# Kernel optimization log

Measured on AMD Instinct MI355X. Metric: run time of the kernel, lower is better.

## Reference

```python
import jax, jax.numpy as jnp
import numpy as np

N = 1_000_000   # samples
D_IN = 100      # covariate dim (cfg_density[0][0])
H = 64          # hidden dim
NUM_HEADS = 5   # t-bins [0,.2,.4,.6,.8,1.0]


def setup_inputs() -> dict:
    key = jax.random.key(0)
    ks = jax.random.split(key, 17)
    s = 0.05  # param scale for numerical stability (torch init is data-independent anyway)
    return {
        "t": jax.random.uniform(ks[0], (N,), dtype=jnp.float32),
        "x": jax.random.normal(ks[1], (N, D_IN), dtype=jnp.float32),
        # density feature MLP (two Linear+ReLU layers)
        "dW1": jax.random.normal(ks[2], (D_IN, H), dtype=jnp.float32) * s,
        "db1": jax.random.normal(ks[3], (H,), dtype=jnp.float32) * s,
        "dW2": jax.random.normal(ks[4], (H, H), dtype=jnp.float32) * s,
        "db2": jax.random.normal(ks[5], (H,), dtype=jnp.float32) * s,
        # 5 multi-head branches, each 3 Treat_Linear layers (istreat=1 since isenhance=1)
        "hw1": jax.random.normal(ks[6], (NUM_HEADS, H, H), dtype=jnp.float32) * s,
        "htw1": jax.random.normal(ks[7], (NUM_HEADS, H), dtype=jnp.float32) * s,
        "hb1": jax.random.normal(ks[8], (NUM_HEADS, H), dtype=jnp.float32) * s,
        "hw2": jax.random.normal(ks[9], (NUM_HEADS, H, H), dtype=jnp.float32) * s,
        "htw2": jax.random.normal(ks[10], (NUM_HEADS, H), dtype=jnp.float32) * s,
        "hb2": jax.random.normal(ks[11], (NUM_HEADS, H), dtype=jnp.float32) * s,
        "hw3": jax.random.normal(ks[12], (NUM_HEADS, H, 1), dtype=jnp.float32) * s,
        "htw3": jax.random.normal(ks[13], (NUM_HEADS, 1), dtype=jnp.float32) * s,
        "hb3": jax.random.normal(ks[14], (NUM_HEADS, 1), dtype=jnp.float32) * s,
    }


def reference(t, x, dW1, db1, dW2, db2,
              hw1, htw1, hb1, hw2, htw2, hb2, hw3, htw3, hb3):
    # hidden_features: Linear+ReLU, Linear+ReLU
    h = jax.nn.relu(x @ dW1 + db1)        # [N, H]
    h = jax.nn.relu(h @ dW2 + db2)        # [N, H]

    tt = t[:, None]                        # treatment column [N, 1]
    # bin index per row: t in [0.2*q, 0.2*(q+1)); last bin closed at 1.0
    bins = jnp.clip(jnp.floor(t * NUM_HEADS).astype(jnp.int32), 0, NUM_HEADS - 1)

    out = jnp.zeros((x.shape[0], 1), dtype=h.dtype)
    for q in range(NUM_HEADS):  # fixed small set of structurally-distinct heads
        # Treat_Linear layer 1: feat@W + t*tw + b, relu
        a = jax.nn.relu(h @ hw1[q] + tt * htw1[q] + hb1[q])
        # Treat_Linear layer 2
        a = jax.nn.relu(a @ hw2[q] + tt * htw2[q] + hb2[q])
        # last layer: no activation, islastlayer=1
        a = a @ hw3[q] + tt * htw3[q] + hb3[q]   # [N, 1]
        out = out + jnp.where((bins == q)[:, None], a, 0.0)
    return out  # Drnet returns (None, Q); g is None so we return Q
```

## Files before the change

### kernel.cpp

```cpp
#include <hip/hip_runtime.h>

typedef _Float16 f16;
typedef _Float16 f16x8 __attribute__((ext_vector_type(8)));
typedef float f32x4 __attribute__((ext_vector_type(4)));

#define NB 5
#define H 64
#define DIN 100
#define NT 256
#define MAIN_BLOCKS 512

#define FR_W1   0
#define FR_W2   1024
#define FR_HD   1536
#define FR_TOT  6656

__global__ __launch_bounds__(256)
void prepack_kernel(const float* __restrict__ dW1, const float* __restrict__ dW2,
                    const float* __restrict__ hw1, const float* __restrict__ hw2,
                    f16x8* __restrict__ pw)
{
    int F = blockIdx.x * 256 + threadIdx.x;
    if (F >= FR_TOT) return;
    int lane = F & 63, g = lane >> 4, c = lane & 15;
    const float* src;
    int s, mt, kmax;
    if (F < FR_W2) {
        int r = F; s = r >> 8; mt = (r >> 6) & 3; src = dW1; kmax = 100;
    } else if (F < FR_HD) {
        int r = F - FR_W2; s = r >> 8; mt = (r >> 6) & 3; src = dW2; kmax = 64;
    } else {
        int r = F - FR_HD; int ql = r >> 9; int q = ql >> 1; int l = ql & 1;
        int r2 = r & 511; s = r2 >> 8; mt = (r2 >> 6) & 3;
        src = (l ? hw2 : hw1) + q * 64 * 64; kmax = 64;
    }
    f16x8 v;
    #pragma unroll
    for (int e = 0; e < 8; ++e) {
        int k = 32 * s + 8 * g + e;
        int m = 16 * mt + c;
        float val = (k < kmax) ? src[k * 64 + m] : 0.0f;
        v[e] = (f16)val;
    }
    pw[F] = v;
}

__device__ __forceinline__ f32x4 mfma16(f16x8 a, f16x8 b, f32x4 c) {
    return __builtin_amdgcn_mfma_f32_16x16x32_f16(a, b, c, 0, 0, 0);
}

__device__ __forceinline__ void epi_plain(unsigned char* buf, int row, int g,
                                          const f32x4* acc, const float* bias) {
    #pragma unroll
    for (int mt = 0; mt < 4; ++mt) {
        const float* bb = &bias[16 * mt + 4 * g];
        union { f16 h[4]; unsigned long long u; } pk;
        #pragma unroll
        for (int r2 = 0; r2 < 4; ++r2) pk.h[r2] = (f16)fmaxf(acc[mt][r2] + bb[r2], 0.f);
        *(unsigned long long*)(buf + ((row * 128 + 32 * mt + 8 * g) ^ ((row & 7) << 4))) = pk.u;
    }
}

__device__ __forceinline__ void epi_t(unsigned char* buf, int row, int g, float rt,
                                      const f32x4* acc, const float* bias, const float* tw) {
    #pragma unroll
    for (int mt = 0; mt < 4; ++mt) {
        const float* bb = &bias[16 * mt + 4 * g];
        const float* tt = &tw[16 * mt + 4 * g];
        union { f16 h[4]; unsigned long long u; } pk;
        #pragma unroll
        for (int r2 = 0; r2 < 4; ++r2)
            pk.h[r2] = (f16)fmaxf(acc[mt][r2] + bb[r2] + rt * tt[r2], 0.f);
        *(unsigned long long*)(buf + ((row * 128 + 32 * mt + 8 * g) ^ ((row & 7) << 4))) = pk.u;
    }
}

__device__ __forceinline__ f16x8 lds_read_h(const unsigned char* buf, int row, int g, int s) {
    return *(const f16x8*)(buf + ((row * 128 + 64 * s + 16 * g) ^ ((row & 7) << 4)));
}

__global__ __launch_bounds__(NT, 2)
void drnet_main(const float* __restrict__ t, const float* __restrict__ x,
                const float* __restrict__ db1, const float* __restrict__ db2,
                const float* __restrict__ hb1, const float* __restrict__ htw1,
                const float* __restrict__ hb2, const float* __restrict__ htw2,
                const float* __restrict__ hw3, const float* __restrict__ htw3,
                const float* __restrict__ hb3,
                const f16x8* __restrict__ pw,
                float* __restrict__ out, int N, int nch)
{
    __shared__ float sb1f[H], sb2f[H];
    __shared__ float shb1[NB * H], shw1t[NB * H], shb2[NB * H], shw2t[NB * H], sw3f[NB * H];
    __shared__ float shtw3[NB], shb3[NB];
    __shared__ unsigned char sli[NT], sqv[NT];
    __shared__ float stv[NT];
    __shared__ float sout[NT];
    __shared__ int scnt[NB + 1], sbase[NB + 1];
    __shared__ __align__(16) unsigned char hbuf[4][2][2][2048];

    const int tid = threadIdx.x;
    const int lane = tid & 63;
    const int wv = tid >> 6;
    const int g = lane >> 4;
    const int row = lane & 15;

    for (int p = tid; p < H; p += NT) { sb1f[p] = db1[p]; sb2f[p] = db2[p]; }
    for (int p = tid; p < NB * H; p += NT) {
        shb1[p] = hb1[p];  shw1t[p] = htw1[p];
        shb2[p] = hb2[p];  shw2t[p] = htw2[p];
        sw3f[p] = hw3[p];
    }
    if (tid < NB) { shtw3[tid] = htw3[tid]; shb3[tid] = hb3[tid]; }

    f16x8 w1f[16], w2f[8];
    #pragma unroll
    for (int u = 0; u < 16; ++u) w1f[u] = pw[FR_W1 + u * 64 + lane];
    #pragma unroll
    for (int u = 0; u < 8; ++u)  w2f[u] = pw[FR_W2 + u * 64 + lane];

    float tpre = 0.f;
    {
        int i0 = blockIdx.x * NT + tid;
        if (blockIdx.x < nch && i0 < N) tpre = t[i0];
    }

    for (int ch = blockIdx.x; ch < nch; ch += MAIN_BLOCKS) {
        if (tid <= NB) scnt[tid] = 0;
        __syncthreads();
        const int i0 = ch * NT + tid;
        const float tv0 = tpre;
        int q0 = NB;
        if (i0 < N) q0 = min((int)(tv0 * 5.0f), NB - 1);
        int pos = atomicAdd(&scnt[q0], 1);
        __syncthreads();
        if (tid == 0) {
            int r = 0;
            #pragma unroll
            for (int b = 0; b <= NB; ++b) { sbase[b] = r; r += scnt[b]; }
        }
        __syncthreads();
        int sp = sbase[q0] + pos;
        sli[sp] = (unsigned char)tid; sqv[sp] = (unsigned char)q0; stv[sp] = tv0;
        __syncthreads();

        {
            int inx = (ch + MAIN_BLOCKS) * NT + tid;
            tpre = (ch + MAIN_BLOCKS < nch && inx < N) ? t[inx] : 0.f;
        }

        for (int j = 0; j < 2; ++j) {
            const int pA = (wv * 4 + 2 * j) * 16;
            const int pB = pA + 16;
            const int qloA = sqv[pA];
            const int qloB = sqv[pB];
            const int liA = sli[pA + row], liB = sli[pB + row];
            const int rqA = sqv[pA + row], rqB = sqv[pB + row];
            const float rtA = stv[pA + row], rtB = stv[pB + row];
            const int ivA = (rqA < NB) ? (ch * NT + liA) : (ch * NT);
            const int ivB = (rqB < NB) ? (ch * NT + liB) : (ch * NT);

            float4 xrA[7], xrB[7];
            {
                const float4* x4 = (const float4*)(x + (size_t)ivA * DIN);
                #pragma unroll
                for (int s = 0; s < 3; ++s) { xrA[2*s] = x4[8*s + 2*g]; xrA[2*s+1] = x4[8*s + 2*g + 1]; }
                xrA[6] = x4[24];
            }
            {
                const float4* x4 = (const float4*)(x + (size_t)ivB * DIN);
                #pragma unroll
                for (int s = 0; s < 3; ++s) { xrB[2*s] = x4[8*s + 2*g]; xrB[2*s+1] = x4[8*s + 2*g + 1]; }
                xrB[6] = x4[24];
            }

            if (qloA >= NB) continue;

            f16x8 xfA[4], xfB[4];
            #pragma unroll
            for (int s = 0; s < 3; ++s) {
                float4 a = xrA[2*s], b = xrA[2*s+1];
                xfA[s][0]=(f16)a.x; xfA[s][1]=(f16)a.y; xfA[s][2]=(f16)a.z; xfA[s][3]=(f16)a.w;
                xfA[s][4]=(f16)b.x; xfA[s][5]=(f16)b.y; xfA[s][6]=(f16)b.z; xfA[s][7]=(f16)b.w;
                float4 c = xrB[2*s], d = xrB[2*s+1];
                xfB[s][0]=(f16)c.x; xfB[s][1]=(f16)c.y; xfB[s][2]=(f16)c.z; xfB[s][3]=(f16)c.w;
                xfB[s][4]=(f16)d.x; xfB[s][5]=(f16)d.y; xfB[s][6]=(f16)d.z; xfB[s][7]=(f16)d.w;
            }
            {
                const bool lo = (g == 0);
                float4 a = xrA[6], b = xrB[6];
                xfA[3][0]=lo?(f16)a.x:(f16)0.f; xfA[3][1]=lo?(f16)a.y:(f16)0.f;
                xfA[3][2]=lo?(f16)a.z:(f16)0.f; xfA[3][3]=lo?(f16)a.w:(f16)0.f;
                xfA[3][4]=(f16)0.f; xfA[3][5]=(f16)0.f; xfA[3][6]=(f16)0.f; xfA[3][7]=(f16)0.f;
                xfB[3][0]=lo?(f16)b.x:(f16)0.f; xfB[3][1]=lo?(f16)b.y:(f16)0.f;
                xfB[3][2]=lo?(f16)b.z:(f16)0.f; xfB[3][3]=lo?(f16)b.w:(f16)0.f;
                xfB[3][4]=(f16)0.f; xfB[3][5]=(f16)0.f; xfB[3][6]=(f16)0.f; xfB[3][7]=(f16)0.f;
            }

            const f32x4 zero = {0.f, 0.f, 0.f, 0.f};
            unsigned char* hA_A = hbuf[wv][0][0];
            unsigned char* hB_A = hbuf[wv][0][1];
            unsigned char* hA_B = hbuf[wv][1][0];
            unsigned char* hB_B = hbuf[wv][1][1];

            f32x4 accA[4] = {zero, zero, zero, zero};
            f32x4 accB[4] = {zero, zero, zero, zero};
            #pragma unroll
            for (int s = 0; s < 4; ++s)
                #pragma unroll
                for (int mt = 0; mt < 4; ++mt) {
                    accA[mt] = mfma16(w1f[s * 4 + mt], xfA[s], accA[mt]);
                    accB[mt] = mfma16(w1f[s * 4 + mt], xfB[s], accB[mt]);
                }
            epi_plain(hA_A, row, g, accA, sb1f);
            epi_plain(hA_B, row, g, accB, sb1f);

            f32x4 acc2A[4] = {zero, zero, zero, zero};
            f32x4 acc2B[4] = {zero, zero, zero, zero};
            #pragma unroll
            for (int s = 0; s < 2; ++s) {
                f16x8 hfA = lds_read_h(hA_A, row, g, s);
                f16x8 hfB = lds_read_h(hA_B, row, g, s);
                #pragma unroll
                for (int mt = 0; mt < 4; ++mt) {
                    acc2A[mt] = mfma16(w2f[s * 4 + mt], hfA, acc2A[mt]);
                    acc2B[mt] = mfma16(w2f[s * 4 + mt], hfB, acc2B[mt]);
                }
            }
            epi_plain(hB_A, row, g, acc2A, sb2f);
            epi_plain(hB_B, row, g, acc2B, sb2f);

            const int qhiA = min((int)sqv[pA + 15], NB - 1);
            int qhi = qhiA;
            if (qloB < NB) qhi = max(qhi, min((int)sqv[pB + 15], NB - 1));

            #pragma unroll 1
            for (int q = qloA; q <= qhi; ++q) {
                const f16x8* ph1 = pw + FR_HD + (q * 2 + 0) * 512;
                const f16x8* ph2 = pw + FR_HD + (q * 2 + 1) * 512;

                f32x4 a1A[4] = {zero, zero, zero, zero};
                f32x4 a1B[4] = {zero, zero, zero, zero};
                #pragma unroll
                for (int s = 0; s < 2; ++s) {
                    f16x8 hfA = lds_read_h(hB_A, row, g, s);
                    f16x8 hfB = lds_read_h(hB_B, row, g, s);
                    #pragma unroll
                    for (int mt = 0; mt < 4; ++mt) {
                        f16x8 wf = ph1[(s * 4 + mt) * 64 + lane];
                        a1A[mt] = mfma16(wf, hfA, a1A[mt]);
                        a1B[mt] = mfma16(wf, hfB, a1B[mt]);
                    }
                }
                epi_t(hA_A, row, g, rtA, a1A, &shb1[q * 64], &shw1t[q * 64]);
                epi_t(hA_B, row, g, rtB, a1B, &shb1[q * 64], &shw1t[q * 64]);

                f32x4 a2A[4] = {zero, zero, zero, zero};
                f32x4 a2B[4] = {zero, zero, zero, zero};
                #pragma unroll
                for (int s = 0; s < 2; ++s) {
                    f16x8 hfA = lds_read_h(hA_A, row, g, s);
                    f16x8 hfB = lds_read_h(hA_B, row, g, s);
                    #pragma unroll
                    for (int mt = 0; mt < 4; ++mt) {
                        f16x8 wf = ph2[(s * 4 + mt) * 64 + lane];
                        a2A[mt] = mfma16(wf, hfA, a2A[mt]);
                        a2B[mt] = mfma16(wf, hfB, a2B[mt]);
                    }
                }

                float pa = 0.f, pb = 0.f;
                #pragma unroll
                for (int mt = 0; mt < 4; ++mt) {
                    const float* bb = &shb2[q * 64 + 16 * mt + 4 * g];
                    const float* tw = &shw2t[q * 64 + 16 * mt + 4 * g];
                    const float* w3 = &sw3f[q * 64 + 16 * mt + 4 * g];
                    #pragma unroll
                    for (int r2 = 0; r2 < 4; ++r2) {
                        float vA = fmaxf(a2A[mt][r2] + bb[r2] + rtA * tw[r2], 0.f);
                        float vB = fmaxf(a2B[mt][r2] + bb[r2] + rtB * tw[r2], 0.f);
                        pa += vA * w3[r2];
                        pb += vB * w3[r2];
                    }
                }
                pa += __shfl_xor(pa, 16, 64);
                pa += __shfl_xor(pa, 32, 64);
                pb += __shfl_xor(pb, 16, 64);
                pb += __shfl_xor(pb, 32, 64);
                if (lane < 16) {
                    if (rqA == q) sout[liA] = pa + rtA * shtw3[q] + shb3[q];
                    if (rqB == q) sout[liB] = pb + rtB * shtw3[q] + shb3[q];
                }
            }
        }

        __syncthreads();
        {
            const int iw = ch * NT + tid;
            if (iw < N) out[iw] = sout[tid];
        }
    }
}

extern "C" void kernel_launch(void* const* d_in, const int* in_sizes, int n_in,
                              void* d_out, int out_size, void* d_ws, size_t ws_size,
                              hipStream_t stream) {
    const float* t    = (const float*)d_in[0];
    const float* x    = (const float*)d_in[1];
    const float* dW1  = (const float*)d_in[2];
    const float* db1  = (const float*)d_in[3];
    const float* dW2  = (const float*)d_in[4];
    const float* db2  = (const float*)d_in[5];
    const float* hw1  = (const float*)d_in[6];
    const float* htw1 = (const float*)d_in[7];
    const float* hb1  = (const float*)d_in[8];
    const float* hw2  = (const float*)d_in[9];
    const float* htw2 = (const float*)d_in[10];
    const float* hb2  = (const float*)d_in[11];
    const float* hw3  = (const float*)d_in[12];
    const float* htw3 = (const float*)d_in[13];
    const float* hb3  = (const float*)d_in[14];
    float* out = (float*)d_out;

    const int N = in_sizes[0];
    const int nch = (N + NT - 1) / NT;
    f16x8* pw = (f16x8*)d_ws;

    prepack_kernel<<<(FR_TOT + 255) / 256, 256, 0, stream>>>(dW1, dW2, hw1, hw2, pw);
    drnet_main<<<MAIN_BLOCKS, NT, 0, stream>>>(t, x, db1, db2, hb1, htw1, hb2, htw2,
                                               hw3, htw3, hb3, pw, out, N, nch);
}
```

Before: 160.6 us.

## Stage trunk weights in LDS and issue all four x tile loads up front

Trunk weight fragments (W1, W2) are now copied once per block into shared memory and read from LDS, instead of living in 24 f16x8 registers per lane. This frees registers so the kernel can prefetch all four 16-row x tiles per wave before any compute, giving more memory-level parallelism. The cost is 24 KB of extra LDS, which may limit occupancy, plus LDS read traffic inside the MFMA loops. Rows are loaded even for wavefronts whose tiles are empty.

```diff
diff --git a/kernel.cpp b/kernel.cpp
--- a/kernel.cpp
+++ b/kernel.cpp
@@ -14,6 +14,7 @@
 #define FR_W2   1024
 #define FR_HD   1536
 #define FR_TOT  6656
+#define FR_TRUNK 1536
 
 __global__ __launch_bounds__(256)
 void prepack_kernel(const float* __restrict__ dW1, const float* __restrict__ dW2,
@@ -45,8 +46,37 @@
     pw[F] = v;
 }
 
+struct XF { f16x8 v[4]; };
+
 __device__ __forceinline__ f32x4 mfma16(f16x8 a, f16x8 b, f32x4 c) {
     return __builtin_amdgcn_mfma_f32_16x16x32_f16(a, b, c, 0, 0, 0);
+}
+
+__device__ __forceinline__ f16x8 ldw(const unsigned char* swf, int idx) {
+    return *(const f16x8*)(swf + (idx << 4));
+}
+
+__device__ __forceinline__ void load_tile(float4* xr, const float* x, int iv, int g) {
+    const float4* x4 = (const float4*)(x + (size_t)iv * DIN);
+    #pragma unroll
+    for (int s = 0; s < 3; ++s) { xr[2*s] = x4[8*s + 2*g]; xr[2*s+1] = x4[8*s + 2*g + 1]; }
+    xr[6] = x4[24];
+}
+
+__device__ __forceinline__ void conv_tile(XF& xf, const float4* xr, int g) {
+    #pragma unroll
+    for (int s = 0; s < 3; ++s) {
+        float4 a = xr[2*s], b = xr[2*s+1];
+        xf.v[s][0]=(f16)a.x; xf.v[s][1]=(f16)a.y; xf.v[s][2]=(f16)a.z; xf.v[s][3]=(f16)a.w;
+        xf.v[s][4]=(f16)b.x; xf.v[s][5]=(f16)b.y; xf.v[s][6]=(f16)b.z; xf.v[s][7]=(f16)b.w;
+    }
+    {
+        const bool lo = (g == 0);
+        float4 a = xr[6];
+        xf.v[3][0]=lo?(f16)a.x:(f16)0.f; xf.v[3][1]=lo?(f16)a.y:(f16)0.f;
+        xf.v[3][2]=lo?(f16)a.z:(f16)0.f; xf.v[3][3]=lo?(f16)a.w:(f16)0.f;
+        xf.v[3][4]=(f16)0.f; xf.v[3][5]=(f16)0.f; xf.v[3][6]=(f16)0.f; xf.v[3][7]=(f16)0.f;
+    }
 }
 
 __device__ __forceinline__ void epi_plain(unsigned char* buf, int row, int g,
@@ -96,6 +126,7 @@
     __shared__ float stv[NT];
     __shared__ float sout[NT];
     __shared__ int scnt[NB + 1], sbase[NB + 1];
+    __shared__ __align__(16) unsigned char swf[FR_TRUNK * 16];
     __shared__ __align__(16) unsigned char hbuf[4][2][2][2048];
 
     const int tid = threadIdx.x;
@@ -111,18 +142,122 @@
         sw3f[p] = hw3[p];
     }
     if (tid < NB) { shtw3[tid] = htw3[tid]; shb3[tid] = hb3[tid]; }
-
-    f16x8 w1f[16], w2f[8];
-    #pragma unroll
-    for (int u = 0; u < 16; ++u) w1f[u] = pw[FR_W1 + u * 64 + lane];
-    #pragma unroll
-    for (int u = 0; u < 8; ++u)  w2f[u] = pw[FR_W2 + u * 64 + lane];
+    for (int p = tid; p < FR_TRUNK; p += NT)
+        ((float4*)swf)[p] = ((const float4*)pw)[p];
 
     float tpre = 0.f;
     {
         int i0 = blockIdx.x * NT + tid;
         if (blockIdx.x < nch && i0 < N) tpre = t[i0];
     }
+
+    auto compute_pair = [&](const XF& xfA, const XF& xfB, int pA) {
+        const int qloA = sqv[pA];
+        if (qloA >= NB) return;
+        const int pB = pA + 16;
+        const int qloB = sqv[pB];
+        const int liA = sli[pA + row], liB = sli[pB + row];
+        const int rqA = sqv[pA + row], rqB = sqv[pB + row];
+        const float rtA = stv[pA + row], rtB = stv[pB + row];
+
+        const f32x4 zero = {0.f, 0.f, 0.f, 0.f};
+        unsigned char* hA_A = hbuf[wv][0][0];
+        unsigned char* hB_A = hbuf[wv][0][1];
+        unsigned char* hA_B = hbuf[wv][1][0];
+        unsigned char* hB_B = hbuf[wv][1][1];
+
+        f32x4 accA[4] = {zero, zero, zero, zero};
+        f32x4 accB[4] = {zero, zero, zero, zero};
+        #pragma unroll
+        for (int s = 0; s < 4; ++s)
+            #pragma unroll
+            for (int mt = 0; mt < 4; ++mt) {
+                f16x8 wf = ldw(swf, FR_W1 + (s * 4 + mt) * 64 + lane);
+                accA[mt] = mfma16(wf, xfA.v[s], accA[mt]);
+                accB[mt] = mfma16(wf, xfB.v[s], accB[mt]);
+            }
+        epi_plain(hA_A, row, g, accA, sb1f);
+        epi_plain(hA_B, row, g, accB, sb1f);
+
+        f32x4 acc2A[4] = {zero, zero, zero, zero};
+        f32x4 acc2B[4] = {zero, zero, zero, zero};
+        #pragma unroll
+        for (int s = 0; s < 2; ++s) {
+            f16x8 hfA = lds_read_h(hA_A, row, g, s);
+            f16x8 hfB = lds_read_h(hA_B, row, g, s);
+            #pragma unroll
+            for (int mt = 0; mt < 4; ++mt) {
+                f16x8 wf = ldw(swf, FR_W2 + (s * 4 + mt) * 64 + lane);
+                acc2A[mt] = mfma16(wf, hfA, acc2A[mt]);
+                acc2B[mt] = mfma16(wf, hfB, acc2B[mt]);
+            }
+        }
+        epi_plain(hB_A, row, g, acc2A, sb2f);
+        epi_plain(hB_B, row, g, acc2B, sb2f);
+
+        const int qhiA = min((int)sqv[pA + 15], NB - 1);
+        int qhi = qhiA;
+        if (qloB < NB) qhi = max(qhi, min((int)sqv[pB + 15], NB - 1));
+
+        #pragma unroll 1
+        for (int q = qloA; q <= qhi; ++q) {
+            const f16x8* ph1 = pw + FR_HD + (q * 2 + 0) * 512;
+            const f16x8* ph2 = pw + FR_HD + (q * 2 + 1) * 512;
+
+            f32x4 a1A[4] = {zero, zero, zero, zero};
+            f32x4 a1B[4] = {zero, zero, zero, zero};
+            #pragma unroll
+            for (int s = 0; s < 2; ++s) {
+                f16x8 hfA = lds_read_h(hB_A, row, g, s);
+                f16x8 hfB = lds_read_h(hB_B, row, g, s);
+                #pragma unroll
+                for (int mt = 0; mt < 4; ++mt) {
+                    f16x8 wf = ph1[(s * 4 + mt) * 64 + lane];
+                    a1A[mt] = mfma16(wf, hfA, a1A[mt]);
+                    a1B[mt] = mfma16(wf, hfB, a1B[mt]);
+                }
+            }
+            epi_t(hA_A, row, g, rtA, a1A, &shb1[q * 64], &shw1t[q * 64]);
+            epi_t(hA_B, row, g, rtB, a1B, &shb1[q * 64], &shw1t[q * 64]);
+
+            f32x4 a2A[4] = {zero, zero, zero, zero};
+            f32x4 a2B[4] = {zero, zero, zero, zero};
+            #pragma unroll
+            for (int s = 0; s < 2; ++s) {
+                f16x8 hfA = lds_read_h(hA_A, row, g, s);
+                f16x8 hfB = lds_read_h(hA_B, row, g, s);
+                #pragma unroll
+                for (int mt = 0; mt < 4; ++mt) {
+                    f16x8 wf = ph2[(s * 4 + mt) * 64 + lane];
+                    a2A[mt] = mfma16(wf, hfA, a2A[mt]);
+                    a2B[mt] = mfma16(wf, hfB, a2B[mt]);
+                }
+            }
+
+            float pa = 0.f, pb = 0.f;
+            #pragma unroll
+            for (int mt = 0; mt < 4; ++mt) {
+                const float* bb = &shb2[q * 64 + 16 * mt + 4 * g];
+                const float* tw = &shw2t[q * 64 + 16 * mt + 4 * g];
+                const float* w3 = &sw3f[q * 64 + 16 * mt + 4 * g];
+                #pragma unroll
+                for (int r2 = 0; r2 < 4; ++r2) {
+                    float vA = fmaxf(a2A[mt][r2] + bb[r2] + rtA * tw[r2], 0.f);
+                    float vB = fmaxf(a2B[mt][r2] + bb[r2] + rtB * tw[r2], 0.f);
+                    pa += vA * w3[r2];
+                    pb += vB * w3[r2];
+                }
+            }
+            pa += __shfl_xor(pa, 16, 64);
+            pa += __shfl_xor(pa, 32, 64);
+            pb += __shfl_xor(pb, 16, 64);
+            pb += __shfl_xor(pb, 32, 64);
+            if (lane < 16) {
+                if (rqA == q) sout[liA] = pa + rtA * shtw3[q] + shb3[q];
+                if (rqB == q) sout[liB] = pb + rtB * shtw3[q] + shb3[q];
+            }
+        }
+    };
 
     for (int ch = blockIdx.x; ch < nch; ch += MAIN_BLOCKS) {
         if (tid <= NB) scnt[tid] = 0;
@@ -148,150 +283,26 @@
             tpre = (ch + MAIN_BLOCKS < nch && inx < N) ? t[inx] : 0.f;
         }
 
-        for (int j = 0; j < 2; ++j) {
-            const int pA = (wv * 4 + 2 * j) * 16;
-            const int pB = pA + 16;
-            const int qloA = sqv[pA];
-            const int qloB = sqv[pB];
-            const int liA = sli[pA + row], liB = sli[pB + row];
-            const int rqA = sqv[pA + row], rqB = sqv[pB + row];
-            const float rtA = stv[pA + row], rtB = stv[pB + row];
-            const int ivA = (rqA < NB) ? (ch * NT + liA) : (ch * NT);
-            const int ivB = (rqB < NB) ? (ch * NT + liB) : (ch * NT);
-
-            float4 xrA[7], xrB[7];
-            {
-                const float4* x4 = (const float4*)(x + (size_t)ivA * DIN);
-                #pragma unroll
-                for (int s = 0; s < 3; ++s) { xrA[2*s] = x4[8*s + 2*g]; xrA[2*s+1] = x4[8*s + 2*g + 1]; }
-                xrA[6] = x4[24];
-            }
-            {
-                const float4* x4 = (const float4*)(x + (size_t)ivB * DIN);
-                #pragma unroll
-                for (int s = 0; s < 3; ++s) { xrB[2*s] = x4[8*s + 2*g]; xrB[2*s+1] = x4[8*s + 2*g + 1]; }
-                xrB[6] = x4[24];
-            }
-
-            if (qloA >= NB) continue;
-
-            f16x8 xfA[4], xfB[4];
-            #pragma unroll
-            for (int s = 0; s < 3; ++s) {
-                float4 a = xrA[2*s], b = xrA[2*s+1];
-                xfA[s][0]=(f16)a.x; xfA[s][1]=(f16)a.y; xfA[s][2]=(f16)a.z; xfA[s][3]=(f16)a.w;
-                xfA[s][4]=(f16)b.x; xfA[s][5]=(f16)b.y; xfA[s][6]=(f16)b.z; xfA[s][7]=(f16)b.w;
-                float4 c = xrB[2*s], d = xrB[2*s+1];
-                xfB[s][0]=(f16)c.x; xfB[s][1]=(f16)c.y; xfB[s][2]=(f16)c.z; xfB[s][3]=(f16)c.w;
-                xfB[s][4]=(f16)d.x; xfB[s][5]=(f16)d.y; xfB[s][6]=(f16)d.z; xfB[s][7]=(f16)d.w;
-            }
-            {
-                const bool lo = (g == 0);
-                float4 a = xrA[6], b = xrB[6];
-                xfA[3][0]=lo?(f16)a.x:(f16)0.f; xfA[3][1]=lo?(f16)a.y:(f16)0.f;
-                xfA[3][2]=lo?(f16)a.z:(f16)0.f; xfA[3][3]=lo?(f16)a.w:(f16)0.f;
-                xfA[3][4]=(f16)0.f; xfA[3][5]=(f16)0.f; xfA[3][6]=(f16)0.f; xfA[3][7]=(f16)0.f;
-                xfB[3][0]=lo?(f16)b.x:(f16)0.f; xfB[3][1]=lo?(f16)b.y:(f16)0.f;
-                xfB[3][2]=lo?(f16)b.z:(f16)0.f; xfB[3][3]=lo?(f16)b.w:(f16)0.f;
-                xfB[3][4]=(f16)0.f; xfB[3][5]=(f16)0.f; xfB[3][6]=(f16)0.f; xfB[3][7]=(f16)0.f;
-            }
-
-            const f32x4 zero = {0.f, 0.f, 0.f, 0.f};
-            unsigned char* hA_A = hbuf[wv][0][0];
-            unsigned char* hB_A = hbuf[wv][0][1];
-            unsigned char* hA_B = hbuf[wv][1][0];
-            unsigned char* hB_B = hbuf[wv][1][1];
-
-            f32x4 accA[4] = {zero, zero, zero, zero};
-            f32x4 accB[4] = {zero, zero, zero, zero};
-            #pragma unroll
-            for (int s = 0; s < 4; ++s)
-                #pragma unroll
-                for (int mt = 0; mt < 4; ++mt) {
-                    accA[mt] = mfma16(w1f[s * 4 + mt], xfA[s], accA[mt]);
-                    accB[mt] = mfma16(w1f[s * 4 + mt], xfB[s], accB[mt]);
-                }
-            epi_plain(hA_A, row, g, accA, sb1f);
-            epi_plain(hA_B, row, g, accB, sb1f);
-
-            f32x4 acc2A[4] = {zero, zero, zero, zero};
-            f32x4 acc2B[4] = {zero, zero, zero, zero};
-            #pragma unroll
-            for (int s = 0; s < 2; ++s) {
-                f16x8 hfA = lds_read_h(hA_A, row, g, s);
-                f16x8 hfB = lds_read_h(hA_B, row, g, s);
-                #pragma unroll
-                for (int mt = 0; mt < 4; ++mt) {
-                    acc2A[mt] = mfma16(w2f[s * 4 + mt], hfA, acc2A[mt]);
-                    acc2B[mt] = mfma16(w2f[s * 4 + mt], hfB, acc2B[mt]);
-                }
-            }
-            epi_plain(hB_A, row, g, acc2A, sb2f);
-            epi_plain(hB_B, row, g, acc2B, sb2f);
-
-            const int qhiA = min((int)sqv[pA + 15], NB - 1);
-            int qhi = qhiA;
-            if (qloB < NB) qhi = max(qhi, min((int)sqv[pB + 15], NB - 1));
-
-            #pragma unroll 1
-            for (int q = qloA; q <= qhi; ++q) {
-                const f16x8* ph1 = pw + FR_HD + (q * 2 + 0) * 512;
-                const f16x8* ph2 = pw + FR_HD + (q * 2 + 1) * 512;
-
-                f32x4 a1A[4] = {zero, zero, zero, zero};
-                f32x4 a1B[4] = {zero, zero, zero, zero};
-                #pragma unroll
-                for (int s = 0; s < 2; ++s) {
-                    f16x8 hfA = lds_read_h(hB_A, row, g, s);
-                    f16x8 hfB = lds_read_h(hB_B, row, g, s);
-                    #pragma unroll
-                    for (int mt = 0; mt < 4; ++mt) {
-                        f16x8 wf = ph1[(s * 4 + mt) * 64 + lane];
-                        a1A[mt] = mfma16(wf, hfA, a1A[mt]);
-                        a1B[mt] = mfma16(wf, hfB, a1B[mt]);
-                    }
-                }
-                epi_t(hA_A, row, g, rtA, a1A, &shb1[q * 64], &shw1t[q * 64]);
-                epi_t(hA_B, row, g, rtB, a1B, &shb1[q * 64], &shw1t[q * 64]);
-
-                f32x4 a2A[4] = {zero, zero, zero, zero};
-                f32x4 a2B[4] = {zero, zero, zero, zero};
-                #pragma unroll
-                for (int s = 0; s < 2; ++s) {
-                    f16x8 hfA = lds_read_h(hA_A, row, g, s);
-                    f16x8 hfB = lds_read_h(hA_B, row, g, s);
-                    #pragma unroll
-                    for (int mt = 0; mt < 4; ++mt) {
-                        f16x8 wf = ph2[(s * 4 + mt) * 64 + lane];
-                        a2A[mt] = mfma16(wf, hfA, a2A[mt]);
-                        a2B[mt] = mfma16(wf, hfB, a2B[mt]);
-                    }
-                }
-
-                float pa = 0.f, pb = 0.f;
-                #pragma unroll
-                for (int mt = 0; mt < 4; ++mt) {
-                    const float* bb = &shb2[q * 64 + 16 * mt + 4 * g];
-                    const float* tw = &shw2t[q * 64 + 16 * mt + 4 * g];
-                    const float* w3 = &sw3f[q * 64 + 16 * mt + 4 * g];
-                    #pragma unroll
-                    for (int r2 = 0; r2 < 4; ++r2) {
-                        float vA = fmaxf(a2A[mt][r2] + bb[r2] + rtA * tw[r2], 0.f);
-                        float vB = fmaxf(a2B[mt][r2] + bb[r2] + rtB * tw[r2], 0.f);
-                        pa += vA * w3[r2];
-                        pb += vB * w3[r2];
-                    }
-                }
-                pa += __shfl_xor(pa, 16, 64);
-                pa += __shfl_xor(pa, 32, 64);
-                pb += __shfl_xor(pb, 16, 64);
-                pb += __shfl_xor(pb, 32, 64);
-                if (lane < 16) {
-                    if (rqA == q) sout[liA] = pa + rtA * shtw3[q] + shb3[q];
-                    if (rqB == q) sout[liB] = pb + rtB * shtw3[q] + shb3[q];
-                }
-            }
-        }
+        const int tb = wv * 64;
+        int ivs[4];
+        #pragma unroll
+        for (int m = 0; m < 4; ++m) {
+            int pm = tb + m * 16 + row;
+            ivs[m] = (sqv[pm] < NB) ? (ch * NT + sli[pm]) : (ch * NT);
+        }
+        float4 xr0[7], xr1[7], xr2[7], xr3[7];
+        load_tile(xr0, x, ivs[0], g);
+        load_tile(xr1, x, ivs[1], g);
+        load_tile(xr2, x, ivs[2], g);
+        load_tile(xr3, x, ivs[3], g);
+
+        XF xfA, xfB;
+        conv_tile(xfA, xr0, g);
+        conv_tile(xfB, xr1, g);
+        compute_pair(xfA, xfB, tb);
+        conv_tile(xfA, xr2, g);
+        conv_tile(xfB, xr3, g);
+        compute_pair(xfA, xfB, tb + 32);
 
         __syncthreads();
         {
```

Result: faster. 157.0 us (-2.2%).
